# Kernel optimization log

Hardware: AMD Instinct MI355X
Metric: run time of the kernel (lower is better)

## Reference

```python
import jax, jax.numpy as jnp
import numpy as np

C_IN = 256
C_INTER = 128
B, H, W = 8, 64, 64
EPS = 1e-5


def setup_inputs() -> dict:
    key = jax.random.key(0)
    ks = jax.random.split(key, 12)
    s = 0.02
    return {
        "x": jax.random.normal(ks[0], (B, C_IN, H, W), dtype=jnp.float32),
        "bn_gamma": jnp.ones((C_IN,), jnp.float32),
        "bn_beta": jnp.zeros((C_IN,), jnp.float32),
        "bn_mean": jax.random.normal(ks[1], (C_IN,), jnp.float32) * 0.1,
        "bn_var": jnp.abs(jax.random.normal(ks[2], (C_IN,), jnp.float32)) * 0.1 + 1.0,
        "w_g": jax.random.normal(ks[3], (C_INTER, C_IN), jnp.float32) * s,
        "b_g": jnp.zeros((C_INTER,), jnp.float32),
        "w_theta": jax.random.normal(ks[4], (C_INTER, C_IN), jnp.float32) * s,
        "b_theta": jnp.zeros((C_INTER,), jnp.float32),
        "w_phi": jax.random.normal(ks[5], (C_INTER, C_IN), jnp.float32) * s,
        "b_phi": jnp.zeros((C_INTER,), jnp.float32),
        "w_w": jax.random.normal(ks[6], (C_IN, C_INTER), jnp.float32) * s,
        "b_w": jnp.zeros((C_IN,), jnp.float32),
    }


def reference(x, bn_gamma, bn_beta, bn_mean, bn_var,
              w_g, b_g, w_theta, b_theta, w_phi, b_phi, w_w, b_w):
    b, c, h, w = x.shape
    # BatchNorm2d (inference form, running stats) -- self.bn in the original
    scale = bn_gamma * jax.lax.rsqrt(bn_var + EPS)
    xb = x * scale[None, :, None, None] + (bn_beta - bn_mean * scale)[None, :, None, None]
    xf = xb.reshape(b, c, h * w)  # (B, C, N); conv1x1 == channel matmul
    g = jnp.einsum('oc,bcn->bon', w_g, xf) + b_g[None, :, None]          # (B, Ci, N)
    th = jnp.einsum('oc,bcn->bon', w_theta, xf) + b_theta[None, :, None]  # (B, Ci, N)
    ph = jnp.einsum('oc,bcn->bon', w_phi, xf) + b_phi[None, :, None]      # (B, Ci, N)
    f = jnp.einsum('bcn,bcm->bnm', th, ph)  # (B, N, N), NO 1/sqrt(d) scaling
    a = jax.nn.softmax(f, axis=-1)
    y = jnp.einsum('bnm,bcm->bcn', a, g)    # (B, Ci, N)
    wy = jnp.einsum('oc,bcn->bon', w_w, y) + b_w[None, :, None]  # (B, C, N)
    return wy.reshape(b, c, h, w) + x
```

## Files before the change

kernel.cpp:

```cpp
#include <hip/hip_runtime.h>
#include <hip/hip_bf16.h>
#include <stdint.h>

#define BB   8
#define CIN  256
#define CI   128
#define NN   4096
#define EPSV 1e-5f
#define LOG2E 1.44269504088896340736f

typedef __attribute__((ext_vector_type(8))) short bf16x8;
typedef __attribute__((ext_vector_type(4))) short bf16x4;
typedef __attribute__((ext_vector_type(4))) float f32x4;
typedef __attribute__((ext_vector_type(2))) float f32x2;
typedef __attribute__((ext_vector_type(2))) unsigned int u32x2;
typedef __attribute__((ext_vector_type(4))) int i32x4;
typedef __attribute__((ext_vector_type(8))) int i32x8;

static __device__ inline short f2bf(float f) {
    uint32_t u = __builtin_bit_cast(uint32_t, f);
    u += 0x7FFFu + ((u >> 16) & 1u);
    return (short)(u >> 16);
}

static __device__ inline float bf2f(short s) {
    uint32_t u = ((uint32_t)(uint16_t)s) << 16;
    return __builtin_bit_cast(float, u);
}

static __device__ inline uint32_t cvt_pk_bf16(float lo, float hi) {
    uint32_t r;
    asm("v_cvt_pk_bf16_f32 %0, %1, %2" : "=v"(r) : "v"(lo), "v"(hi));
    return r;
}

__global__ __launch_bounds__(256) void prep_kernel(
    const float* __restrict__ wth, const float* __restrict__ wph,
    const float* __restrict__ wg,  const float* __restrict__ ww,
    short* __restrict__ wq, short* __restrict__ wwb)
{
    int t = blockIdx.x * 256 + threadIdx.x;
    if (t < 12288) {
        int s  = t >> 12;
        int r  = t & 4095;
        int o  = r >> 5;
        int j  = r & 31;
        int k  = j >> 3, jj = j & 7;
        const float* W = (s == 0) ? wth : (s == 1) ? wph : wg;
        float sc = (s == 0) ? LOG2E : 1.0f;
        const float* src = &W[(size_t)o * CIN + k * 64 + jj * 8];
        bf16x8 d;
        #pragma unroll
        for (int i = 0; i < 8; ++i) d[i] = f2bf(src[i] * sc);
        size_t doff = (size_t)s * 65536 + (size_t)k * 16384
                    + (size_t)o * 128 + (size_t)((jj ^ (o & 7)) << 4);
        *(bf16x8*)((char*)wq + doff) = d;
    } else if (t < 16384) {
        int r = t - 12288;
        int o = r >> 4, j = r & 15;
        const float* src = &ww[(size_t)o * CI + j * 8];
        bf16x8 d;
        #pragma unroll
        for (int i = 0; i < 8; ++i) d[i] = f2bf(src[i]);
        *(bf16x8*)&wwb[(size_t)o * CI + j * 8] = d;
    }
}

__global__ __launch_bounds__(256, 2) void proj_kernel(
    const float* __restrict__ x,
    const float* __restrict__ gamma, const float* __restrict__ beta,
    const float* __restrict__ mean,  const float* __restrict__ var,
    const short* __restrict__ wq,
    const float* __restrict__ bth, const float* __restrict__ bph,
    const float* __restrict__ bg,
    unsigned char* __restrict__ qp, unsigned char* __restrict__ kp,
    short* __restrict__ vtp)
{
    __shared__ float s_scale[CIN];
    __shared__ float s_shift[CIN];
    __shared__ __align__(16) short A_lds[64][264];
    __shared__ __align__(16) char  B_sh[2][128 * 128];

    const int tid = threadIdx.x;
    const int b   = blockIdx.x & 7;
    const int n0  = (blockIdx.x >> 3) * 64;
    const int w = tid >> 6, lane = tid & 63, lr = lane & 15, lg = lane >> 4;

    {
        float sc = gamma[tid] * rsqrtf(var[tid] + EPSV);
        s_scale[tid] = sc;
        s_shift[tid] = beta[tid] - mean[tid] * sc;
    }
    __syncthreads();

    #pragma unroll
    for (int p = 0; p < 8; ++p) {
        int c2 = p * 32 + (tid >> 4) * 2;
        int n4 = (tid & 15) * 4;
        f32x4 v0 = *(const f32x4*)&x[((size_t)b * CIN + c2) * NN + n0 + n4];
        f32x4 v1 = *(const f32x4*)&x[((size_t)b * CIN + c2 + 1) * NN + n0 + n4];
        float sc0 = s_scale[c2],     sh0 = s_shift[c2];
        float sc1 = s_scale[c2 + 1], sh1 = s_shift[c2 + 1];
        #pragma unroll
        for (int i = 0; i < 4; ++i) {
            uint32_t pk = cvt_pk_bf16(v0[i] * sc0 + sh0, v1[i] * sc1 + sh1);
            *(uint32_t*)&A_lds[n4 + i][c2] = pk;
        }
    }

    auto stageB = [&](int buf, int idx) {
        const char* src = (const char*)wq + (size_t)idx * 16384;
        #pragma unroll
        for (int r = 0; r < 4; ++r) {
            __builtin_amdgcn_global_load_lds(
                (const __attribute__((address_space(1))) void*)
                    (src + ((((r * 4 + w) << 6) + lane) << 4)),
                (__attribute__((address_space(3))) void*)&B_sh[buf][(r * 4 + w) << 10],
                16, 0, 0);
        }
    };
    stageB(0, 0);
    __syncthreads();

    const float* BS[3] = {bth, bph, bg};
    f32x4 acc[8];

    for (int idx = 0; idx < 12; ++idx) {
        const int s = idx >> 2, k = idx & 3, buf = idx & 1;
        if (idx + 1 < 12) stageB(buf ^ 1, idx + 1);

        if (k == 0) {
            #pragma unroll
            for (int i = 0; i < 8; ++i) acc[i] = (f32x4){0.f, 0.f, 0.f, 0.f};
        }
        const int c0 = k * 64;
        bf16x8 a0 = *(const bf16x8*)&A_lds[w * 16 + lr][c0 + lg * 8];
        bf16x8 a1 = *(const bf16x8*)&A_lds[w * 16 + lr][c0 + 32 + lg * 8];
        const char* Bc = B_sh[buf];
        #pragma unroll
        for (int ot = 0; ot < 8; ++ot) {
            const int o  = ot * 16 + lr;
            const int sw = (o & 7) << 4;
            bf16x8 b0 = *(const bf16x8*)(Bc + o * 128 + ((lg << 4) ^ sw));
            bf16x8 b1 = *(const bf16x8*)(Bc + o * 128 + (((4 + lg) << 4) ^ sw));
            acc[ot] = __builtin_amdgcn_mfma_f32_16x16x32_bf16(a0, b0, acc[ot], 0, 0, 0);
            acc[ot] = __builtin_amdgcn_mfma_f32_16x16x32_bf16(a1, b1, acc[ot], 0, 0, 0);
        }

        if (k == 3) {
            if (s < 2) {
                unsigned char* dst = (s == 0) ? qp : kp;
                const float om = (s == 0) ? LOG2E : 1.0f;
                #pragma unroll
                for (int ot = 0; ot < 8; ++ot) {
                    float bias = BS[s][ot * 16 + lr] * om;
                    #pragma unroll
                    for (int rr = 0; rr < 4; ++rr) {
                        int n = n0 + w * 16 + lg * 4 + rr;
                        uint32_t pk = __builtin_amdgcn_cvt_pk_fp8_f32(
                            acc[ot][rr] + bias, 0.f, 0, false);
                        dst[((size_t)b * NN + n) * 128 + ot * 16 + lr] =
                            (unsigned char)(pk & 0xFF);
                    }
                }
            } else {
                #pragma unroll
                for (int ot = 0; ot < 8; ++ot) {
                    float bias = BS[s][ot * 16 + lr];
                    bf16x4 pk;
                    #pragma unroll
                    for (int rr = 0; rr < 4; ++rr) pk[rr] = f2bf(acc[ot][rr] + bias);
                    *(bf16x4*)&vtp[((size_t)b * CI + ot * 16 + lr) * NN + n0 + w * 16 + lg * 4] = pk;
                }
            }
        }
        __syncthreads();
    }
}

__global__ __launch_bounds__(256, 2) void attn_kernel(
    const unsigned char* __restrict__ qp, const unsigned char* __restrict__ kp,
    const short* __restrict__ vtp, short* __restrict__ yh,
    float* __restrict__ ml)
{
    __shared__ __align__(16) char K_sh[2][64 * 128];
    __shared__ __align__(16) char V_sh[2][128 * 128];
    __shared__ __align__(16) char P_sh[4][16 * 128];

    const int tid  = threadIdx.x;
    const int b    = blockIdx.x & 7;
    const int half = (blockIdx.x >> 3) & 1;
    const int n0   = (blockIdx.x >> 4) * 128;
    const int w = tid >> 6, lane = tid & 63, lr = lane & 15, lg = lane >> 4;
    const int NT = NN / 128;
    const int t0 = half * NT;

    const unsigned char* kgp[2];
    const char* vgp[4];
    #pragma unroll
    for (int r = 0; r < 2; ++r) {
        int idx = ((r * 4 + w) << 6) + lane;
        int mm  = idx >> 3, cb = (idx & 7) << 4;
        kgp[r] = kp + (size_t)b * NN * 128 + (size_t)(t0 * 64 + mm) * 128
               + (cb ^ ((mm & 7) << 4));
    }
    #pragma unroll
    for (int r = 0; r < 4; ++r) {
        int idx = ((r * 4 + w) << 6) + lane;
        int cc = idx >> 3, cbv = (idx & 7) << 4;
        vgp[r] = (const char*)(vtp + (size_t)b * CI * NN + (size_t)t0 * 64
                               + (size_t)cc * NN) + (cbv ^ ((cc & 7) << 4));
    }
    auto stage = [&](int bufi) {
        #pragma unroll
        for (int r = 0; r < 2; ++r) {
            __builtin_amdgcn_global_load_lds(
                (const __attribute__((address_space(1))) void*)kgp[r],
                (__attribute__((address_space(3))) void*)&K_sh[bufi][(r * 4 + w) << 10],
                16, 0, 0);
            kgp[r] += 64 * 128;
        }
        #pragma unroll
        for (int r = 0; r < 4; ++r) {
            __builtin_amdgcn_global_load_lds(
                (const __attribute__((address_space(1))) void*)vgp[r],
                (__attribute__((address_space(3))) void*)&V_sh[bufi][(r * 4 + w) << 10],
                16, 0, 0);
            vgp[r] += 64 * 2;
        }
    };

    i32x8 qf8[2];
    #pragma unroll
    for (int s = 0; s < 2; ++s) {
        const unsigned char* qrow = qp + ((size_t)b * NN + n0 + w * 32 + s * 16 + lr) * 128;
        i32x4 lo = *(const i32x4*)(qrow + lg * 32);
        i32x4 hi = *(const i32x4*)(qrow + lg * 32 + 16);
        qf8[s] = (i32x8){lo[0], lo[1], lo[2], lo[3], hi[0], hi[1], hi[2], hi[3]};
    }

    f32x4 yacc[2][8];
    #pragma unroll
    for (int s = 0; s < 2; ++s)
        #pragma unroll
        for (int i = 0; i < 8; ++i) yacc[s][i] = (f32x4){0.f, 0.f, 0.f, 0.f};
    float m_run[2] = {-__builtin_huge_valf(), -__builtin_huge_valf()};
    float l_run[2] = {0.f, 0.f};

    stage(0);
    __syncthreads();

    for (int t = 0; t < NT; ++t) {
        const int cur = t & 1;
        if (t + 1 < NT) stage(cur ^ 1);

        const char* Kc = K_sh[cur];
        f32x4 sa[2][4];
        __builtin_amdgcn_s_setprio(1);
        #pragma unroll
        for (int mt = 0; mt < 4; ++mt) {
            const int mrow = mt * 16 + lr;
            const int sw   = (mrow & 7) << 4;
            const char* kr = Kc + mrow * 128;
            i32x4 k0 = *(const i32x4*)(kr + ((lg * 32) ^ sw));
            i32x4 k1 = *(const i32x4*)(kr + ((lg * 32 + 16) ^ sw));
            i32x8 kf8 = (i32x8){k0[0], k0[1], k0[2], k0[3], k1[0], k1[1], k1[2], k1[3]};
            sa[0][mt] = __builtin_amdgcn_mfma_scale_f32_16x16x128_f8f6f4(
                kf8, qf8[0], (f32x4){0.f, 0.f, 0.f, 0.f},
                0, 0, 0, 0x7F7F7F7F, 0, 0x7F7F7F7F);
            sa[1][mt] = __builtin_amdgcn_mfma_scale_f32_16x16x128_f8f6f4(
                kf8, qf8[1], (f32x4){0.f, 0.f, 0.f, 0.f},
                0, 0, 0, 0x7F7F7F7F, 0, 0x7F7F7F7F);
        }
        __builtin_amdgcn_s_setprio(0);

        float tml[2];
        #pragma unroll
        for (int s = 0; s < 2; ++s) {
            float tm = fmaxf(fmaxf(fmaxf(sa[s][0][0], sa[s][0][1]), fmaxf(sa[s][0][2], sa[s][0][3])),
                             fmaxf(fmaxf(sa[s][1][0], sa[s][1][1]), fmaxf(sa[s][1][2], sa[s][1][3])));
            tm = fmaxf(tm, fmaxf(fmaxf(fmaxf(sa[s][2][0], sa[s][2][1]), fmaxf(sa[s][2][2], sa[s][2][3])),
                                 fmaxf(fmaxf(sa[s][3][0], sa[s][3][1]), fmaxf(sa[s][3][2], sa[s][3][3]))));
            tml[s] = tm;
        }
        if (__any((tml[0] - m_run[0] > 8.f) || (tml[1] - m_run[1] > 8.f))) {
            #pragma unroll
            for (int s = 0; s < 2; ++s) {
                float tm = tml[s];
                tm = fmaxf(tm, __shfl_xor(tm, 16));
                tm = fmaxf(tm, __shfl_xor(tm, 32));
                float mnew = fmaxf(m_run[s], tm);
                float sc   = __builtin_amdgcn_exp2f(m_run[s] - mnew);
                m_run[s] = mnew;
                l_run[s] *= sc;
                #pragma unroll
                for (int rr = 0; rr < 4; ++rr) {
                    float scb = __shfl(sc, (lane & 48) | (lg * 4 + rr));
                    #pragma unroll
                    for (int ct = 0; ct < 8; ++ct) yacc[s][ct][rr] *= scb;
                }
            }
        }

        const char* Vc = V_sh[cur];
        bf16x8 vf[2][8];
        #pragma unroll
        for (int kf = 0; kf < 2; ++kf)
            #pragma unroll
            for (int ct = 0; ct < 8; ++ct) {
                const int vr = ct * 16 + lr;
                vf[kf][ct] = *(const bf16x8*)(Vc + (vr << 7) +
                                              ((kf * 64 + lg * 16) ^ ((vr & 7) << 4)));
            }

        char* Pb = P_sh[w];
        const int psw = (lr & 7) << 4;
        bf16x8 pa0[2], pa1[2];
        {
            float rs = 0.f;
            #pragma unroll
            for (int mt = 0; mt < 4; ++mt) {
                float e0 = __builtin_amdgcn_exp2f(sa[0][mt][0] - m_run[0]);
                float e1 = __builtin_amdgcn_exp2f(sa[0][mt][1] - m_run[0]);
                float e2 = __builtin_amdgcn_exp2f(sa[0][mt][2] - m_run[0]);
                float e3 = __builtin_amdgcn_exp2f(sa[0][mt][3] - m_run[0]);
                rs += (e0 + e1) + (e2 + e3);
                u32x2 pk = {cvt_pk_bf16(e0, e1), cvt_pk_bf16(e2, e3)};
                *(u32x2*)(Pb + lr * 128 + ((mt * 32 + lg * 8) ^ psw)) = pk;
            }
            l_run[0] += rs;
        }
        asm volatile("" ::: "memory");
        #pragma unroll
        for (int kf = 0; kf < 2; ++kf)
            pa0[kf] = *(const bf16x8*)(Pb + lr * 128 + ((kf * 64 + lg * 16) ^ psw));
        asm volatile("" ::: "memory");

        {
            float rs = 0.f;
            #pragma unroll
            for (int mt = 0; mt < 4; ++mt) {
                float e0 = __builtin_amdgcn_exp2f(sa[1][mt][0] - m_run[1]);
                float e1 = __builtin_amdgcn_exp2f(sa[1][mt][1] - m_run[1]);
                float e2 = __builtin_amdgcn_exp2f(sa[1][mt][2] - m_run[1]);
                float e3 = __builtin_amdgcn_exp2f(sa[1][mt][3] - m_run[1]);
                rs += (e0 + e1) + (e2 + e3);
                u32x2 pk = {cvt_pk_bf16(e0, e1), cvt_pk_bf16(e2, e3)};
                *(u32x2*)(Pb + lr * 128 + ((mt * 32 + lg * 8) ^ psw)) = pk;
            }
            l_run[1] += rs;
        }
        asm volatile("" ::: "memory");
        #pragma unroll
        for (int kf = 0; kf < 2; ++kf)
            pa1[kf] = *(const bf16x8*)(Pb + lr * 128 + ((kf * 64 + lg * 16) ^ psw));

        __builtin_amdgcn_s_setprio(1);
        #pragma unroll
        for (int kf = 0; kf < 2; ++kf)
            #pragma unroll
            for (int ct = 0; ct < 8; ++ct) {
                yacc[0][ct] = __builtin_amdgcn_mfma_f32_16x16x32_bf16(pa0[kf], vf[kf][ct], yacc[0][ct], 0, 0, 0);
                yacc[1][ct] = __builtin_amdgcn_mfma_f32_16x16x32_bf16(pa1[kf], vf[kf][ct], yacc[1][ct], 0, 0, 0);
            }
        __builtin_amdgcn_s_setprio(0);

        __syncthreads();
    }

    #pragma unroll
    for (int s = 0; s < 2; ++s) {
        float lt = l_run[s];
        lt += __shfl_xor(lt, 16);
        lt += __shfl_xor(lt, 32);
        l_run[s] = lt;
    }

    short* yb = yh + ((size_t)half * BB + b) * NN * (size_t)CI;
    #pragma unroll
    for (int s = 0; s < 2; ++s) {
        #pragma unroll
        for (int rr = 0; rr < 4; ++rr) {
            int n = n0 + w * 32 + s * 16 + lg * 4 + rr;
            #pragma unroll
            for (int ct = 0; ct < 8; ++ct)
                yb[(size_t)n * CI + ct * 16 + lr] = f2bf(yacc[s][ct][rr]);
        }
    }
    if (lg == 0) {
        #pragma unroll
        for (int s = 0; s < 2; ++s) {
            int n = n0 + w * 32 + s * 16 + lr;
            f32x2 v = {m_run[s], l_run[s]};
            *(f32x2*)&ml[(((size_t)half * BB + b) * NN + n) * 2] = v;
        }
    }
}

__global__ __launch_bounds__(256) void merge_kernel(
    const short* __restrict__ yh, const float* __restrict__ ml,
    short* __restrict__ yp)
{
    const int tid = threadIdx.x;
    const int row = blockIdx.x * 8 + (tid >> 5);
    const int c4  = (tid & 31) * 4;
    const size_t H = (size_t)BB * NN * CI;
    const size_t R = (size_t)BB * NN * 2;

    float m0 = ml[(size_t)row * 2],     l0 = ml[(size_t)row * 2 + 1];
    float m1 = ml[R + (size_t)row * 2], l1 = ml[R + (size_t)row * 2 + 1];
    float mm = fmaxf(m0, m1);
    float w0 = __builtin_amdgcn_exp2f(m0 - mm);
    float w1 = __builtin_amdgcn_exp2f(m1 - mm);
    float inv = 1.0f / (l0 * w0 + l1 * w1);
    w0 *= inv; w1 *= inv;

    bf16x4 a  = *(const bf16x4*)&yh[(size_t)row * CI + c4];
    bf16x4 bb = *(const bf16x4*)&yh[H + (size_t)row * CI + c4];
    bf16x4 o;
    #pragma unroll
    for (int i = 0; i < 4; ++i) o[i] = f2bf(bf2f(a[i]) * w0 + bf2f(bb[i]) * w1);
    *(bf16x4*)&yp[(size_t)row * CI + c4] = o;
}

template <int MERGED>
__global__ __launch_bounds__(256) void out_kernel(
    const short* __restrict__ ysrc, const float* __restrict__ ml,
    const short* __restrict__ wwb, const float* __restrict__ bw,
    const float* __restrict__ x, float* __restrict__ out)
{
    __shared__ __align__(16) short A_lds[128][136];
    __shared__ __align__(16) short Bl[128][136];

    const int tid  = threadIdx.x;
    const int b    = blockIdx.x & 7;
    const int rest = blockIdx.x >> 3;
    const int ob   = rest & 1;
    const int nn   = (rest >> 1) * 128;
    const int o0   = ob * 128;
    const int w = tid >> 6, lane = tid & 63, lr = lane & 15, lg = lane >> 4;

    #pragma unroll
    for (int pass = 0; pass < 8; ++pass) {
        int o  = pass * 16 + (tid >> 4);
        int c8 = (tid & 15) * 8;
        *(bf16x8*)&A_lds[o][c8] = *(const bf16x8*)&wwb[(size_t)(o0 + o) * CI + c8];
    }
    #pragma unroll
    for (int pass = 0; pass < 8; ++pass) {
        int n  = pass * 16 + (tid >> 4);
        int c8 = (tid & 15) * 8;
        size_t row = (size_t)b * NN + nn + n;
        if (MERGED) {
            *(bf16x8*)&Bl[n][c8] = *(const bf16x8*)&ysrc[row * CI + c8];
        } else {
            const size_t H = (size_t)BB * NN * CI;
            const size_t R = (size_t)BB * NN * 2;
            f32x2 v0 = *(const f32x2*)&ml[row * 2];
            f32x2 v1 = *(const f32x2*)&ml[R + row * 2];
            float mm = fmaxf(v0[0], v1[0]);
            float w0 = __builtin_amdgcn_exp2f(v0[0] - mm);
            float w1 = __builtin_amdgcn_exp2f(v1[0] - mm);
            float inv = 1.0f / (v0[1] * w0 + v1[1] * w1);
            w0 *= inv; w1 *= inv;
            bf16x8 a  = *(const bf16x8*)&ysrc[row * CI + c8];
            bf16x8 b2 = *(const bf16x8*)&ysrc[H + row * CI + c8];
            bf16x8 ov;
            #pragma unroll
            for (int i = 0; i < 4; ++i) {
                float lo = bf2f(a[2*i]) * w0 + bf2f(b2[2*i]) * w1;
                float hi = bf2f(a[2*i+1]) * w0 + bf2f(b2[2*i+1]) * w1;
                uint32_t pk = cvt_pk_bf16(lo, hi);
                ov[2*i]   = (short)(pk & 0xFFFF);
                ov[2*i+1] = (short)(pk >> 16);
            }
            *(bf16x8*)&Bl[n][c8] = ov;
        }
    }
    __syncthreads();

    f32x4 acc[2][8];
    #pragma unroll
    for (int i = 0; i < 2; ++i)
        #pragma unroll
        for (int j = 0; j < 8; ++j) acc[i][j] = (f32x4){0.f, 0.f, 0.f, 0.f};

    #pragma unroll
    for (int kf = 0; kf < 4; ++kf) {
        bf16x8 a0 = *(const bf16x8*)&A_lds[w * 32 + lr][kf * 32 + lg * 8];
        bf16x8 a1 = *(const bf16x8*)&A_lds[w * 32 + 16 + lr][kf * 32 + lg * 8];
        #pragma unroll
        for (int nt = 0; nt < 8; ++nt) {
            bf16x8 bv = *(const bf16x8*)&Bl[nt * 16 + lr][kf * 32 + lg * 8];
            acc[0][nt] = __builtin_amdgcn_mfma_f32_16x16x32_bf16(a0, bv, acc[0][nt], 0, 0, 0);
            acc[1][nt] = __builtin_amdgcn_mfma_f32_16x16x32_bf16(a1, bv, acc[1][nt], 0, 0, 0);
        }
    }

    #pragma unroll
    for (int wo = 0; wo < 2; ++wo) {
        #pragma unroll
        for (int rr = 0; rr < 4; ++rr) {
            int o = o0 + w * 32 + wo * 16 + lg * 4 + rr;
            float bias = bw[o];
            #pragma unroll
            for (int nt = 0; nt < 8; ++nt) {
                size_t idx = ((size_t)b * CIN + o) * NN + nn + nt * 16 + lr;
                out[idx] = acc[wo][nt][rr] + bias + x[idx];
            }
        }
    }
}

extern "C" void kernel_launch(void* const* d_in, const int* in_sizes, int n_in,
                              void* d_out, int out_size, void* d_ws, size_t ws_size,
                              hipStream_t stream)
{
    const float* x     = (const float*)d_in[0];
    const float* gamma = (const float*)d_in[1];
    const float* beta  = (const float*)d_in[2];
    const float* mean  = (const float*)d_in[3];
    const float* var   = (const float*)d_in[4];
    const float* wg    = (const float*)d_in[5];
    const float* bg    = (const float*)d_in[6];
    const float* wth   = (const float*)d_in[7];
    const float* bth   = (const float*)d_in[8];
    const float* wph   = (const float*)d_in[9];
    const float* bph   = (const float*)d_in[10];
    const float* ww    = (const float*)d_in[11];
    const float* bw    = (const float*)d_in[12];

    const size_t seg = (size_t)BB * NN * CI;
    unsigned char* qp = (unsigned char*)d_ws;
    unsigned char* kp = (unsigned char*)d_ws + seg * sizeof(short);
    short* vtp = (short*)((char*)d_ws + 2 * seg * sizeof(short));
    float* ml  = (float*)((char*)d_ws + 3 * seg * sizeof(short));
    short* wq  = (short*)((char*)d_ws + 25690112);
    short* wwb = (short*)((char*)d_ws + 25690112 + 196608);
    const size_t yh_off = 25u * 1024 * 1024;
    const bool fused = ws_size >= yh_off + 2 * seg * sizeof(short);
    short* yh = fused ? (short*)((char*)d_ws + yh_off) : (short*)d_out;
    (void)in_sizes; (void)n_in; (void)out_size;

    prep_kernel<<<64, 256, 0, stream>>>(wth, wph, wg, ww, wq, wwb);
    proj_kernel<<<BB * (NN / 64), 256, 0, stream>>>(
        x, gamma, beta, mean, var, wq, bth, bph, bg, qp, kp, vtp);
    attn_kernel<<<2 * BB * (NN / 128), 256, 0, stream>>>(qp, kp, vtp, yh, ml);
    if (fused) {
        out_kernel<0><<<2 * BB * (NN / 128), 256, 0, stream>>>(
            yh, ml, wwb, bw, x, (float*)d_out);
    } else {
        short* yp = (short*)d_ws;
        merge_kernel<<<BB * NN / 8, 256, 0, stream>>>(yh, ml, yp);
        out_kernel<1><<<2 * BB * (NN / 128), 256, 0, stream>>>(
            yp, ml, wwb, bw, x, (float*)d_out);
    }
}
```

Measured before the change: 103.5 us.

## Store V and softmax probabilities in FP8 and use FP8 MFMA for PV

```diff
diff --git a/kernel.cpp b/kernel.cpp
--- a/kernel.cpp
+++ b/kernel.cpp
@@ -74,7 +74,7 @@
     const float* __restrict__ bth, const float* __restrict__ bph,
     const float* __restrict__ bg,
     unsigned char* __restrict__ qp, unsigned char* __restrict__ kp,
-    short* __restrict__ vtp)
+    unsigned char* __restrict__ vt8)
 {
     __shared__ float s_scale[CIN];
     __shared__ float s_shift[CIN];
@@ -167,10 +167,12 @@
                 #pragma unroll
                 for (int ot = 0; ot < 8; ++ot) {
                     float bias = BS[s][ot * 16 + lr];
-                    bf16x4 pk;
-                    #pragma unroll
-                    for (int rr = 0; rr < 4; ++rr) pk[rr] = f2bf(acc[ot][rr] + bias);
-                    *(bf16x4*)&vtp[((size_t)b * CI + ot * 16 + lr) * NN + n0 + w * 16 + lg * 4] = pk;
+                    uint32_t d = __builtin_amdgcn_cvt_pk_fp8_f32(
+                        acc[ot][0] + bias, acc[ot][1] + bias, 0, false);
+                    d = __builtin_amdgcn_cvt_pk_fp8_f32(
+                        acc[ot][2] + bias, acc[ot][3] + bias, d, true);
+                    *(uint32_t*)&vt8[((size_t)b * CI + ot * 16 + lr) * NN
+                                     + n0 + w * 16 + lg * 4] = d;
                 }
             }
         }
@@ -180,12 +182,12 @@
 
 __global__ __launch_bounds__(256, 2) void attn_kernel(
     const unsigned char* __restrict__ qp, const unsigned char* __restrict__ kp,
-    const short* __restrict__ vtp, short* __restrict__ yh,
+    const unsigned char* __restrict__ vt8, short* __restrict__ yh,
     float* __restrict__ ml)
 {
     __shared__ __align__(16) char K_sh[2][64 * 128];
     __shared__ __align__(16) char V_sh[2][128 * 128];
-    __shared__ __align__(16) char P_sh[4][16 * 128];
+    __shared__ __align__(16) char P_sh[4][2][16 * 128];
 
     const int tid  = threadIdx.x;
     const int b    = blockIdx.x & 7;
@@ -196,7 +198,7 @@
     const int t0 = half * NT;
 
     const unsigned char* kgp[2];
-    const char* vgp[4];
+    const unsigned char* vgp[4];
     #pragma unroll
     for (int r = 0; r < 2; ++r) {
         int idx = ((r * 4 + w) << 6) + lane;
@@ -208,10 +210,10 @@
     for (int r = 0; r < 4; ++r) {
         int idx = ((r * 4 + w) << 6) + lane;
         int cc = idx >> 3, cbv = (idx & 7) << 4;
-        vgp[r] = (const char*)(vtp + (size_t)b * CI * NN + (size_t)t0 * 64
-                               + (size_t)cc * NN) + (cbv ^ ((cc & 7) << 4));
-    }
-    auto stage = [&](int bufi) {
+        vgp[r] = vt8 + (size_t)b * CI * NN + (size_t)cc * NN + t0 * 64
+               + (cbv ^ ((cc & 7) << 4));
+    }
+    auto stageK = [&](int bufi) {
         #pragma unroll
         for (int r = 0; r < 2; ++r) {
             __builtin_amdgcn_global_load_lds(
@@ -220,13 +222,15 @@
                 16, 0, 0);
             kgp[r] += 64 * 128;
         }
+    };
+    auto stageV = [&](int bufi) {
         #pragma unroll
         for (int r = 0; r < 4; ++r) {
             __builtin_amdgcn_global_load_lds(
                 (const __attribute__((address_space(1))) void*)vgp[r],
                 (__attribute__((address_space(3))) void*)&V_sh[bufi][(r * 4 + w) << 10],
                 16, 0, 0);
-            vgp[r] += 64 * 2;
+            vgp[r] += 128;
         }
     };
 
@@ -247,14 +251,19 @@
     float m_run[2] = {-__builtin_huge_valf(), -__builtin_huge_valf()};
     float l_run[2] = {0.f, 0.f};
 
-    stage(0);
+    stageK(0);
+    stageV(0);
     __syncthreads();
 
+    const int psw = (lr & 7) << 4;
+
     for (int t = 0; t < NT; ++t) {
-        const int cur = t & 1;
-        if (t + 1 < NT) stage(cur ^ 1);
-
-        const char* Kc = K_sh[cur];
+        const int kcur = t & 1;
+        if (t + 1 < NT) stageK(kcur ^ 1);
+        const int p = t >> 1;
+        if ((t & 1) == 0 && p + 1 < NT / 2) stageV((p & 1) ^ 1);
+
+        const char* Kc = K_sh[kcur];
         f32x4 sa[2][4];
         __builtin_amdgcn_s_setprio(1);
         #pragma unroll
@@ -274,96 +283,80 @@
         }
         __builtin_amdgcn_s_setprio(0);
 
-        float tml[2];
+        if ((t & 1) == 0) {
+            float tml[2];
+            #pragma unroll
+            for (int s = 0; s < 2; ++s) {
+                float tm = fmaxf(fmaxf(fmaxf(sa[s][0][0], sa[s][0][1]), fmaxf(sa[s][0][2], sa[s][0][3])),
+                                 fmaxf(fmaxf(sa[s][1][0], sa[s][1][1]), fmaxf(sa[s][1][2], sa[s][1][3])));
+                tm = fmaxf(tm, fmaxf(fmaxf(fmaxf(sa[s][2][0], sa[s][2][1]), fmaxf(sa[s][2][2], sa[s][2][3])),
+                                     fmaxf(fmaxf(sa[s][3][0], sa[s][3][1]), fmaxf(sa[s][3][2], sa[s][3][3]))));
+                tml[s] = tm;
+            }
+            if (__any((tml[0] - m_run[0] > 4.f) || (tml[1] - m_run[1] > 4.f))) {
+                #pragma unroll
+                for (int s = 0; s < 2; ++s) {
+                    float tm = tml[s];
+                    tm = fmaxf(tm, __shfl_xor(tm, 16));
+                    tm = fmaxf(tm, __shfl_xor(tm, 32));
+                    float mnew = fmaxf(m_run[s], tm);
+                    float sc   = __builtin_amdgcn_exp2f(m_run[s] - mnew);
+                    m_run[s] = mnew;
+                    l_run[s] *= sc;
+                    #pragma unroll
+                    for (int rr = 0; rr < 4; ++rr) {
+                        float scb = __shfl(sc, (lane & 48) | (lg * 4 + rr));
+                        #pragma unroll
+                        for (int ct = 0; ct < 8; ++ct) yacc[s][ct][rr] *= scb;
+                    }
+                }
+            }
+        }
+
+        const int h64 = (t & 1) << 6;
         #pragma unroll
         for (int s = 0; s < 2; ++s) {
-            float tm = fmaxf(fmaxf(fmaxf(sa[s][0][0], sa[s][0][1]), fmaxf(sa[s][0][2], sa[s][0][3])),
-                             fmaxf(fmaxf(sa[s][1][0], sa[s][1][1]), fmaxf(sa[s][1][2], sa[s][1][3])));
-            tm = fmaxf(tm, fmaxf(fmaxf(fmaxf(sa[s][2][0], sa[s][2][1]), fmaxf(sa[s][2][2], sa[s][2][3])),
-                                 fmaxf(fmaxf(sa[s][3][0], sa[s][3][1]), fmaxf(sa[s][3][2], sa[s][3][3]))));
-            tml[s] = tm;
-        }
-        if (__any((tml[0] - m_run[0] > 8.f) || (tml[1] - m_run[1] > 8.f))) {
+            char* Pb = &P_sh[w][s][0] + lr * 128;
+            float rs = 0.f;
+            #pragma unroll
+            for (int mt = 0; mt < 4; ++mt) {
+                float e0 = __builtin_amdgcn_exp2f(sa[s][mt][0] - m_run[s]);
+                float e1 = __builtin_amdgcn_exp2f(sa[s][mt][1] - m_run[s]);
+                float e2 = __builtin_amdgcn_exp2f(sa[s][mt][2] - m_run[s]);
+                float e3 = __builtin_amdgcn_exp2f(sa[s][mt][3] - m_run[s]);
+                rs += (e0 + e1) + (e2 + e3);
+                uint32_t d = __builtin_amdgcn_cvt_pk_fp8_f32(e0, e1, 0, false);
+                d = __builtin_amdgcn_cvt_pk_fp8_f32(e2, e3, d, true);
+                *(uint32_t*)(Pb + ((h64 + mt * 16 + lg * 4) ^ psw)) = d;
+            }
+            l_run[s] += rs;
+        }
+
+        if (t & 1) {
+            asm volatile("" ::: "memory");
+            i32x8 pa8[2];
             #pragma unroll
             for (int s = 0; s < 2; ++s) {
-                float tm = tml[s];
-                tm = fmaxf(tm, __shfl_xor(tm, 16));
-                tm = fmaxf(tm, __shfl_xor(tm, 32));
-                float mnew = fmaxf(m_run[s], tm);
-                float sc   = __builtin_amdgcn_exp2f(m_run[s] - mnew);
-                m_run[s] = mnew;
-                l_run[s] *= sc;
-                #pragma unroll
-                for (int rr = 0; rr < 4; ++rr) {
-                    float scb = __shfl(sc, (lane & 48) | (lg * 4 + rr));
-                    #pragma unroll
-                    for (int ct = 0; ct < 8; ++ct) yacc[s][ct][rr] *= scb;
-                }
-            }
-        }
-
-        const char* Vc = V_sh[cur];
-        bf16x8 vf[2][8];
-        #pragma unroll
-        for (int kf = 0; kf < 2; ++kf)
+                const char* Pb = &P_sh[w][s][0] + lr * 128;
+                i32x4 p0 = *(const i32x4*)(Pb + ((lg * 32) ^ psw));
+                i32x4 p1 = *(const i32x4*)(Pb + ((lg * 32 + 16) ^ psw));
+                pa8[s] = (i32x8){p0[0], p0[1], p0[2], p0[3], p1[0], p1[1], p1[2], p1[3]};
+            }
+            const char* Vc = V_sh[p & 1];
+            __builtin_amdgcn_s_setprio(1);
             #pragma unroll
             for (int ct = 0; ct < 8; ++ct) {
-                const int vr = ct * 16 + lr;
-                vf[kf][ct] = *(const bf16x8*)(Vc + (vr << 7) +
-                                              ((kf * 64 + lg * 16) ^ ((vr & 7) << 4)));
-            }
-
-        char* Pb = P_sh[w];
-        const int psw = (lr & 7) << 4;
-        bf16x8 pa0[2], pa1[2];
-        {
-            float rs = 0.f;
-            #pragma unroll
-            for (int mt = 0; mt < 4; ++mt) {
-                float e0 = __builtin_amdgcn_exp2f(sa[0][mt][0] - m_run[0]);
-                float e1 = __builtin_amdgcn_exp2f(sa[0][mt][1] - m_run[0]);
-                float e2 = __builtin_amdgcn_exp2f(sa[0][mt][2] - m_run[0]);
-                float e3 = __builtin_amdgcn_exp2f(sa[0][mt][3] - m_run[0]);
-                rs += (e0 + e1) + (e2 + e3);
-                u32x2 pk = {cvt_pk_bf16(e0, e1), cvt_pk_bf16(e2, e3)};
-                *(u32x2*)(Pb + lr * 128 + ((mt * 32 + lg * 8) ^ psw)) = pk;
-            }
-            l_run[0] += rs;
-        }
-        asm volatile("" ::: "memory");
-        #pragma unroll
-        for (int kf = 0; kf < 2; ++kf)
-            pa0[kf] = *(const bf16x8*)(Pb + lr * 128 + ((kf * 64 + lg * 16) ^ psw));
-        asm volatile("" ::: "memory");
-
-        {
-            float rs = 0.f;
-            #pragma unroll
-            for (int mt = 0; mt < 4; ++mt) {
-                float e0 = __builtin_amdgcn_exp2f(sa[1][mt][0] - m_run[1]);
-                float e1 = __builtin_amdgcn_exp2f(sa[1][mt][1] - m_run[1]);
-                float e2 = __builtin_amdgcn_exp2f(sa[1][mt][2] - m_run[1]);
-                float e3 = __builtin_amdgcn_exp2f(sa[1][mt][3] - m_run[1]);
-                rs += (e0 + e1) + (e2 + e3);
-                u32x2 pk = {cvt_pk_bf16(e0, e1), cvt_pk_bf16(e2, e3)};
-                *(u32x2*)(Pb + lr * 128 + ((mt * 32 + lg * 8) ^ psw)) = pk;
-            }
-            l_run[1] += rs;
-        }
-        asm volatile("" ::: "memory");
-        #pragma unroll
-        for (int kf = 0; kf < 2; ++kf)
-            pa1[kf] = *(const bf16x8*)(Pb + lr * 128 + ((kf * 64 + lg * 16) ^ psw));
-
-        __builtin_amdgcn_s_setprio(1);
-        #pragma unroll
-        for (int kf = 0; kf < 2; ++kf)
-            #pragma unroll
-            for (int ct = 0; ct < 8; ++ct) {
-                yacc[0][ct] = __builtin_amdgcn_mfma_f32_16x16x32_bf16(pa0[kf], vf[kf][ct], yacc[0][ct], 0, 0, 0);
-                yacc[1][ct] = __builtin_amdgcn_mfma_f32_16x16x32_bf16(pa1[kf], vf[kf][ct], yacc[1][ct], 0, 0, 0);
-            }
-        __builtin_amdgcn_s_setprio(0);
+                const char* vrow = Vc + (ct * 16 + lr) * 128;
+                i32x4 v0 = *(const i32x4*)(vrow + ((lg * 32) ^ psw));
+                i32x4 v1 = *(const i32x4*)(vrow + ((lg * 32 + 16) ^ psw));
+                i32x8 vf8 = (i32x8){v0[0], v0[1], v0[2], v0[3], v1[0], v1[1], v1[2], v1[3]};
+                yacc[0][ct] = __builtin_amdgcn_mfma_scale_f32_16x16x128_f8f6f4(
+                    pa8[0], vf8, yacc[0][ct], 0, 0, 0, 0x7F7F7F7F, 0, 0x7F7F7F7F);
+                yacc[1][ct] = __builtin_amdgcn_mfma_scale_f32_16x16x128_f8f6f4(
+                    pa8[1], vf8, yacc[1][ct], 0, 0, 0, 0x7F7F7F7F, 0, 0x7F7F7F7F);
+            }
+            __builtin_amdgcn_s_setprio(0);
+        }
 
         __syncthreads();
     }
@@ -531,9 +524,9 @@
     const float* bw    = (const float*)d_in[12];
 
     const size_t seg = (size_t)BB * NN * CI;
-    unsigned char* qp = (unsigned char*)d_ws;
-    unsigned char* kp = (unsigned char*)d_ws + seg * sizeof(short);
-    short* vtp = (short*)((char*)d_ws + 2 * seg * sizeof(short));
+    unsigned char* qp  = (unsigned char*)d_ws;
+    unsigned char* kp  = (unsigned char*)d_ws + seg * sizeof(short);
+    unsigned char* vt8 = (unsigned char*)d_ws + 2 * seg * sizeof(short);
     float* ml  = (float*)((char*)d_ws + 3 * seg * sizeof(short));
     short* wq  = (short*)((char*)d_ws + 25690112);
     short* wwb = (short*)((char*)d_ws + 25690112 + 196608);
@@ -544,8 +537,8 @@
 
     prep_kernel<<<64, 256, 0, stream>>>(wth, wph, wg, ww, wq, wwb);
     proj_kernel<<<BB * (NN / 64), 256, 0, stream>>>(
-        x, gamma, beta, mean, var, wq, bth, bph, bg, qp, kp, vtp);
-    attn_kernel<<<2 * BB * (NN / 128), 256, 0, stream>>>(qp, kp, vtp, yh, ml);
+        x, gamma, beta, mean, var, wq, bth, bph, bg, qp, kp, vt8);
+    attn_kernel<<<2 * BB * (NN / 128), 256, 0, stream>>>(qp, kp, vt8, yh, ml);
     if (fused) {
         out_kernel<0><<<2 * BB * (NN / 128), 256, 0, stream>>>(
             yh, ml, wwb, bw, x, (float*)d_out);
```

After: 100.8 us. 1.03x faster.
